# Performance work log

Measured on AMD Instinct MI355X. Metric: run time of the kernel, lower is better.

Reference implementation:

```python
import jax, jax.numpy as jnp
import numpy as np

B, C_IN, C_OUT, N, T = 32, 64, 192, 307, 24
DILATIONS = (1, 2)
O3 = C_OUT // 3  # out channels per branch


def setup_inputs() -> dict:
    key = jax.random.key(0)
    ks = iter(jax.random.split(key, 32))
    nrm = lambda shape: 0.05 * jax.random.normal(next(ks), shape, dtype=jnp.float32)
    return {
        "x": jax.random.normal(next(ks), (B, C_IN, N, T), dtype=jnp.float32),
        "adj": jax.random.randint(next(ks), (N, N), 0, 2, dtype=jnp.int32),
        "ln_g": jnp.ones((T,), jnp.float32),
        "ln_b": jnp.zeros((T,), jnp.float32),
        "res_W": nrm((C_OUT, C_IN)), "res_b": nrm((C_OUT,)),
        "ca_W1": nrm((T,)), "ca_W2": nrm((N, T)), "ca_W3": nrm((N,)),
        "cc_W": nrm((O3, C_IN)), "cc_b": nrm((O3,)),
        "ta_W1": nrm((N,)), "ta_W2": nrm((C_IN, N)), "ta_W3": nrm((C_IN,)),
        "tc_W0": nrm((O3, C_IN, 1, 2)), "tc_b0": nrm((O3,)),
        "tc_W1": nrm((O3, O3, 1, 2)), "tc_b1": nrm((O3,)),
        "ga_W1": nrm((T,)), "ga_W2": nrm((C_IN, T)), "ga_W3": nrm((C_IN,)),
        "g_W": nrm((O3, C_IN)),
    }


def layer_norm_lastdim(x, g, b, eps=1e-5):
    mu = jnp.mean(x, axis=-1, keepdims=True)
    var = jnp.var(x, axis=-1, keepdims=True)
    return (x - mu) * jax.lax.rsqrt(var + eps) * g + b


def conv1x1(x, W, b):
    # x: [B,C,N,T], W: [O,C]
    return jnp.einsum("oc,bcnt->bont", W, x) + b[None, :, None, None]


def c_attention(x, W1, W2, W3):
    # channel attention over C; x: [B,C,N,T]
    lhs = jnp.einsum("bcn,nt->bct", jnp.einsum("bcnt,t->bcn", x, W1), W2)  # [B,C,T]
    rhs = jnp.einsum("n,bcnt->bct", W3, x)                                  # [B,C,T]
    att = jax.nn.softmax(jnp.einsum("bct,bdt->bcd", lhs, rhs), axis=-1)     # [B,C,C]
    return jnp.einsum("bcd,bdnt->bcnt", att, x)


def t_attention(x, W1, W2, W3):
    # temporal attention over T; x: [B,C,N,T]
    lhs = jnp.einsum("bct,cn->btn", jnp.einsum("bcnt,n->bct", x, W1), W2)   # [B,T,N]
    rhs = jnp.einsum("c,bcnt->bnt", W3, x)                                   # [B,N,T]
    att = jax.nn.softmax(jnp.einsum("btn,bns->bts", lhs, rhs), axis=-1)      # [B,T,T]
    return jnp.einsum("bts,bcns->bcnt", att, x)


def g_attention(x, adj, W1, W2, W3):
    # graph (spatial) attention over N, masked by adjacency; x: [B,C,N,T]
    lhs = jnp.einsum("bcn,ct->bnt", jnp.einsum("bcnt,t->bcn", x, W1), W2)   # [B,N,T]
    rhs = jnp.einsum("c,bcnt->bnt", W3, x)                                   # [B,N,T]
    scores = jnp.einsum("bnt,bmt->bnm", lhs, rhs)                            # [B,N,N]
    scores = jnp.where(adj[None] > 0, scores, jnp.float32(-1e30))
    att = jax.nn.softmax(scores, axis=-1)
    return jnp.einsum("bnm,bcmt->bcnt", att, x)


def causal_conv(x, W, b, d):
    # Conv2d kernel [1,2], dilation [1,d], pad [0,d] + Chomp(d) == left-pad-only causal conv
    y = jax.lax.conv_general_dilated(
        x, W, window_strides=(1, 1), padding=((0, 0), (d, 0)),
        rhs_dilation=(1, d), dimension_numbers=("NCHW", "OIHW", "NCHW"))
    return y + b[None, :, None, None]


def meam_forward(x, adj, ln_g, ln_b, res_W, res_b, ca_W1, ca_W2, ca_W3, cc_W, cc_b,
                 ta_W1, ta_W2, ta_W3, tc_W0, tc_b0, tc_W1, tc_b1,
                 ga_W1, ga_W2, ga_W3, g_W):
    h = layer_norm_lastdim(x, ln_g, ln_b)
    # CACN branch: channel attention + 1x1 conv
    c_out = conv1x1(c_attention(h, ca_W1, ca_W2, ca_W3), cc_W, cc_b)
    # TACN branch: temporal attention + dilated causal convs
    t_out = t_attention(h, ta_W1, ta_W2, ta_W3)
    t_out = causal_conv(t_out, tc_W0, tc_b0, DILATIONS[0])
    t_out = causal_conv(t_out, tc_W1, tc_b1, DILATIONS[1])
    # GACN branch: graph attention + channel mixing
    g_out = jnp.einsum("oc,bcnt->bont", g_W, g_attention(h, adj, ga_W1, ga_W2, ga_W3))
    out = jnp.concatenate([c_out, t_out, g_out], axis=1)  # [B, C_OUT, N, T]
    return jax.nn.relu(out + conv1x1(x, res_W, res_b))


def reference(x, adj, ln_g, ln_b, res_W, res_b, ca_W1, ca_W2, ca_W3, cc_W, cc_b,
              ta_W1, ta_W2, ta_W3, tc_W0, tc_b0, tc_W1, tc_b1,
              ga_W1, ga_W2, ga_W3, g_W):
    return meam_forward(x, adj, ln_g, ln_b, res_W, res_b, ca_W1, ca_W2, ca_W3, cc_W, cc_b,
                        ta_W1, ta_W2, ta_W3, tc_W0, tc_b0, tc_W1, tc_b1,
                        ga_W1, ga_W2, ga_W3, g_W)
```

## Files before the change

### kernel.cpp

```cpp
#include <hip/hip_runtime.h>
#include <hip/hip_bf16.h>

#define BB 32
#define CC 64
#define NN 307
#define TT 24
#define CO 192
#define NT (NN*TT)
#define GO 1536

using bf16 = __hip_bfloat16;
typedef __attribute__((ext_vector_type(8))) short bf16x8;
typedef __attribute__((ext_vector_type(4))) float f32x4;

#define OFF_ln_g   0
#define OFF_ln_b   24
#define OFF_res_W  48
#define OFF_res_b  12336
#define OFF_ca_W1  12528
#define OFF_ca_W2  12552
#define OFF_ca_W3  19920
#define OFF_cc_W   20227
#define OFF_cc_b   24323
#define OFF_ta_W1  24387
#define OFF_ta_W2  24694
#define OFF_ta_W3  44342
#define OFF_tc_W0  44406
#define OFF_tc_b0  52598
#define OFF_tc_W1  52662
#define OFF_tc_b1  60854
#define OFF_ga_W1  60918
#define OFF_ga_W2  60942
#define OFF_ga_W3  62478
#define OFF_g_W    62542
#define W_TOTAL    66638

__device__ __forceinline__ float xload(const void* p, size_t i, int f) {
  return f ? ((const float*)p)[i] : __bfloat162float(((const bf16*)p)[i]);
}
__device__ __forceinline__ void ostore(void* p, size_t i, float v, int f) {
  if (f) ((float*)p)[i] = v; else ((bf16*)p)[i] = __float2bfloat16(v);
}
__device__ __forceinline__ float oload(const void* p, size_t i, int f) {
  return f ? ((const float*)p)[i] : __bfloat162float(((const bf16*)p)[i]);
}

__global__ void MEAM_44787918963464_kernel() {}

__global__ __launch_bounds__(256) void k_probe(const void* lng_raw, int* flag) {
  if (threadIdx.x == 0 && blockIdx.x == 0) {
    unsigned w = *(const unsigned*)lng_raw;
    *flag = (w == 0x3F800000u) ? 1 : 0;
  }
}

__global__ __launch_bounds__(256) void k_cvt_w(
    const void* p0, const void* p1, const void* p2, const void* p3,
    const void* p4, const void* p5, const void* p6, const void* p7,
    const void* p8, const void* p9, const void* p10, const void* p11,
    const void* p12, const void* p13, const void* p14, const void* p15,
    const void* p16, const void* p17, const void* p18, const void* p19,
    const int* flagp, float* dst) {
  int i = blockIdx.x*256 + threadIdx.x;
  if (i >= W_TOTAL) return;
  const void* ps[20] = {p0,p1,p2,p3,p4,p5,p6,p7,p8,p9,p10,p11,p12,p13,p14,p15,p16,p17,p18,p19};
  const int sz[20] = {24,24,12288,192,24,7368,307,4096,64,307,19648,64,8192,64,8192,64,24,1536,64,4096};
  int f = *flagp;
  int s = 0, base = 0;
  while (i >= base + sz[s]) { base += sz[s]; s++; }
  dst[i] = f ? ((const float*)ps[s])[i-base]
             : __bfloat162float(((const bf16*)ps[s])[i-base]);
}

__global__ __launch_bounds__(256) void k_prep_tc(const float* __restrict__ W,
    bf16* __restrict__ Ag, float* __restrict__ tb_bias) {
  int g = blockIdx.x*256 + threadIdx.x;
  if (g >= CC*CC) return;
  int pI = g >> 6, c = g & 63;
  const float* W0 = W + OFF_tc_W0;
  const float* b0 = W + OFF_tc_b0;
  const float* W1 = W + OFF_tc_W1;
  const float* b1 = W + OFF_tc_b1;
  const float* resW = W + OFF_res_W;
  const float* resb = W + OFF_res_b;
  float m0=0.f,m1=0.f,m2=0.f,m3=0.f, bb0=0.f, bb2=0.f;
  for (int o=0;o<CC;o++){
    float a1v = W1[(pI*CC+o)*2], b1v = W1[(pI*CC+o)*2+1];
    float a0v = W0[(o*CC+c)*2],  b0v = W0[(o*CC+c)*2+1];
    m0 += b1v*b0v; m1 += b1v*a0v; m2 += a1v*b0v; m3 += a1v*a0v;
    bb0 += b1v*b0[o]; bb2 += a1v*b0[o];
  }
  Ag[pI*320 + 0*64 + c] = __float2bfloat16(m0);
  Ag[pI*320 + 1*64 + c] = __float2bfloat16(m1);
  Ag[pI*320 + 2*64 + c] = __float2bfloat16(m2);
  Ag[pI*320 + 3*64 + c] = __float2bfloat16(m3);
  Ag[pI*320 + 4*64 + c] = __float2bfloat16(resW[(64+pI)*CC + c]);
  if (c == 0){
    tb_bias[pI]    = b1[pI] + bb0 + resb[64+pI];
    tb_bias[64+pI] = bb2;
  }
}

__global__ __launch_bounds__(256) void k_prep_A(const float* __restrict__ Mc,
    const float* __restrict__ W, bf16* __restrict__ Apre) {
  int idx = blockIdx.x*256 + threadIdx.x;
  if (idx >= BB*192*128) return;
  int b = idx / 24576;
  int rem = idx - b*24576;
  int p2 = rem >> 7, k = rem & 127;
  const float* resW = W + OFF_res_W;
  const float* gW   = W + OFF_g_W;
  float v;
  if (p2 < 64)       v = (k < 64) ? Mc[b*CC*CC + p2*CC + k] : resW[p2*CC + (k-64)];
  else if (p2 < 128) v = (k < 64) ? gW[(p2-64)*CC + k] : 0.f;
  else               v = (k < 64) ? 0.f : resW[p2*CC + (k-64)];
  Apre[idx] = __float2bfloat16(v);
}

__global__ __launch_bounds__(256) void k_ln(const void* __restrict__ x, const int* flagp,
    const float* __restrict__ W,
    float* __restrict__ mu_o, float* __restrict__ rs_o,
    float* __restrict__ xw1c, float* __restrict__ xw1g) {
  int r = blockIdx.x*256 + threadIdx.x;
  if (r >= BB*CC*NN) return;
  int f = *flagp;
  const float* lng  = W + OFF_ln_g;
  const float* lnb  = W + OFF_ln_b;
  const float* caW1 = W + OFF_ca_W1;
  const float* gaW1 = W + OFF_ga_W1;
  float v[TT];
  float mu = 0.f;
  for (int t=0;t<TT;t++){ v[t] = xload(x, (size_t)r*TT+t, f); mu += v[t]; }
  mu *= (1.f/TT);
  float var = 0.f;
  for (int t=0;t<TT;t++){ float d=v[t]-mu; var += d*d; }
  var *= (1.f/TT);
  float rs = rsqrtf(var + 1e-5f);
  float s1=0.f, s2=0.f;
  for (int t=0;t<TT;t++){
    float hv = (v[t]-mu)*rs*lng[t] + lnb[t];
    s1 += hv*caW1[t];
    s2 += hv*gaW1[t];
  }
  mu_o[r]=mu; rs_o[r]=rs; xw1c[r]=s1; xw1g[r]=s2;
}

__global__ __launch_bounds__(256) void k_prep_ct(const void* __restrict__ x, const int* flagp,
    const float* __restrict__ mu_a, const float* __restrict__ rs_a,
    const float* __restrict__ W, const float* __restrict__ xw1c,
    float* __restrict__ lhsc, float* __restrict__ rhsc, float* __restrict__ xw1t) {
  int i = blockIdx.x*256 + threadIdx.x;
  if (i >= BB*CC*TT) return;
  int f = *flagp;
  const float* lng  = W + OFF_ln_g;
  const float* lnb  = W + OFF_ln_b;
  const float* caW2 = W + OFF_ca_W2;
  const float* caW3 = W + OFF_ca_W3;
  const float* taW1 = W + OFF_ta_W1;
  int t = i % TT; int bc = i / TT;
  float gt = lng[t], bt = lnb[t];
  float l=0.f, rr=0.f, xt=0.f;
  for (int n=0;n<NN;n++){
    int row = bc*NN + n;
    float hv = (xload(x, (size_t)row*TT+t, f) - mu_a[row]) * rs_a[row] * gt + bt;
    l  += xw1c[row]*caW2[n*TT+t];
    rr += caW3[n]*hv;
    xt += taW1[n]*hv;
  }
  lhsc[i]=l; rhsc[i]=rr; xw1t[i]=xt;
}

__global__ __launch_bounds__(256) void k_prep_bn(const void* __restrict__ x, const int* flagp,
    const float* __restrict__ mu_a, const float* __restrict__ rs_a,
    const float* __restrict__ W, const float* __restrict__ xw1g,
    float* __restrict__ rhst, float* __restrict__ rhsg, float* __restrict__ lhsg) {
  int i = blockIdx.x*256 + threadIdx.x;
  if (i >= BB*NN*TT) return;
  int f = *flagp;
  const float* lng  = W + OFF_ln_g;
  const float* lnb  = W + OFF_ln_b;
  const float* taW3 = W + OFF_ta_W3;
  const float* gaW3 = W + OFF_ga_W3;
  const float* gaW2 = W + OFF_ga_W2;
  int t = i % TT; int n = (i/TT)%NN; int b = i/(NN*TT);
  float gt = lng[t], bt = lnb[t];
  float a=0.f,c2=0.f,d=0.f;
  for (int c=0;c<CC;c++){
    int row = (b*CC+c)*NN + n;
    float hv = (xload(x, (size_t)row*TT+t, f) - mu_a[row]) * rs_a[row] * gt + bt;
    a  += taW3[c]*hv;
    c2 += gaW3[c]*hv;
    d  += xw1g[row]*gaW2[c*TT+t];
  }
  rhst[i]=a; rhsg[i]=c2; lhsg[i]=d;
}

__global__ __launch_bounds__(256) void k_lhs_t(const float* __restrict__ xw1t,
    const float* __restrict__ W, float* __restrict__ lhst) {
  int i = blockIdx.x*256 + threadIdx.x;
  if (i >= BB*TT*NN) return;
  const float* taW2 = W + OFF_ta_W2;
  int n = i % NN; int t = (i/NN)%TT; int b = i/(TT*NN);
  float acc=0.f;
  for (int c=0;c<CC;c++)
    acc += xw1t[(b*CC+c)*TT+t]*taW2[c*NN+n];
  lhst[i]=acc;
}

__global__ __launch_bounds__(256) void k_att_c(const float* __restrict__ lhsc,
    const float* __restrict__ rhsc, const float* __restrict__ W,
    float* __restrict__ Mc) {
  int b = blockIdx.x; int tid = threadIdx.x;
  const float* ccW = W + OFF_cc_W;
  __shared__ float lc[CC*TT], rc[CC*TT], sc[CC*(CC+1)];
  for (int e=tid;e<CC*TT;e+=256){
    lc[e]=lhsc[b*CC*TT+e];
    rc[e]=rhsc[b*CC*TT+e];
  }
  __syncthreads();
  for (int e=tid;e<CC*CC;e+=256){
    int c=e>>6, d=e&63; float s=0.f;
    for (int t=0;t<TT;t++) s += lc[c*TT+t]*rc[d*TT+t];
    sc[c*(CC+1)+d]=s;
  }
  __syncthreads();
  if (tid<CC){
    float mx=-1e30f;
    for (int d=0;d<CC;d++) mx=fmaxf(mx, sc[tid*(CC+1)+d]);
    float sum=0.f;
    for (int d=0;d<CC;d++){ float e2=__expf(sc[tid*(CC+1)+d]-mx); sc[tid*(CC+1)+d]=e2; sum+=e2; }
    float inv=1.f/sum;
    for (int d=0;d<CC;d++) sc[tid*(CC+1)+d]*=inv;
  }
  __syncthreads();
  for (int e=tid;e<CC*CC;e+=256){
    int o=e>>6, d=e&63; float acc=0.f;
    for (int c=0;c<CC;c++) acc += ccW[o*CC+c]*sc[c*(CC+1)+d];
    Mc[b*CC*CC+e]=acc;
  }
}

__global__ __launch_bounds__(256) void k_att_t(const float* __restrict__ lhst,
    const float* __restrict__ rhst, float* __restrict__ attt) {
  int b=blockIdx.x, tid=threadIdx.x;
  __shared__ float sc[TT*TT];
  for (int e=tid;e<TT*TT;e+=256){
    int t=e/TT, s=e%TT;
    float acc=0.f;
    for (int n=0;n<NN;n++)
      acc += lhst[(b*TT+t)*NN+n]*rhst[(b*NN+n)*TT+s];
    sc[e]=acc;
  }
  __syncthreads();
  if (tid < TT){
    float mx=-1e30f;
    for (int s=0;s<TT;s++) mx=fmaxf(mx,sc[tid*TT+s]);
    float sum=0.f;
    for (int s=0;s<TT;s++){ float e=__expf(sc[tid*TT+s]-mx); sc[tid*TT+s]=e; sum+=e; }
    float inv=1.f/sum;
    for (int s=0;s<TT;s++) attt[b*TT*TT + tid*TT + s]=sc[tid*TT+s]*inv;
  }
}

__global__ __launch_bounds__(256) void k_scores_g(const float* __restrict__ lhsg,
    const float* __restrict__ rhsg, const int* __restrict__ adj,
    float* __restrict__ Sg) {
  int mt = blockIdx.x, nt = blockIdx.y, b = blockIdx.z;
  int n0 = nt*64, m0 = mt*64, tid = threadIdx.x;
  __shared__ unsigned short Lh[64*40], Ll[64*40], Rh[64*40], Rl[64*40];
  for (int e=tid; e<64*24; e+=256){
    int r=e/24, t=e-(e/24)*24;
    int gn=n0+r, gm=m0+r;
    float lv = (gn<NN)? lhsg[((size_t)b*NN+gn)*TT+t] : 0.f;
    float rv = (gm<NN)? rhsg[((size_t)b*NN+gm)*TT+t] : 0.f;
    bf16 lh=__float2bfloat16(lv); float lhf=__bfloat162float(lh);
    bf16 llo=__float2bfloat16(lv-lhf);
    bf16 rh=__float2bfloat16(rv); float rhf=__bfloat162float(rh);
    bf16 rlo=__float2bfloat16(rv-rhf);
    Lh[r*40+t]=*(unsigned short*)&lh; Ll[r*40+t]=*(unsigned short*)&llo;
    Rh[r*40+t]=*(unsigned short*)&rh; Rl[r*40+t]=*(unsigned short*)&rlo;
  }
  for (int e=tid; e<64*8; e+=256){
    int r=e>>3, t=24+(e&7);
    Lh[r*40+t]=0; Ll[r*40+t]=0; Rh[r*40+t]=0; Rl[r*40+t]=0;
  }
  __syncthreads();
  int lane=tid&63, w=tid>>6, q=lane>>4, lr=lane&15;
  bf16x8 ah = *(const bf16x8*)&Lh[(w*16+lr)*40 + q*8];
  bf16x8 al = *(const bf16x8*)&Ll[(w*16+lr)*40 + q*8];
  f32x4 z4={0.f,0.f,0.f,0.f};
  f32x4 acc[4]={z4,z4,z4,z4};
  #pragma unroll
  for (int ct=0;ct<4;ct++){
    bf16x8 bh = *(const bf16x8*)&Rh[(ct*16+lr)*40 + q*8];
    bf16x8 bl = *(const bf16x8*)&Rl[(ct*16+lr)*40 + q*8];
    acc[ct]=__builtin_amdgcn_mfma_f32_16x16x32_bf16(ah,bh,acc[ct],0,0,0);
    acc[ct]=__builtin_amdgcn_mfma_f32_16x16x32_bf16(ah,bl,acc[ct],0,0,0);
    acc[ct]=__builtin_amdgcn_mfma_f32_16x16x32_bf16(al,bh,acc[ct],0,0,0);
  }
  #pragma unroll
  for (int ct=0;ct<4;ct++){
    int m = m0 + ct*16 + lr;
    #pragma unroll
    for (int r=0;r<4;r++){
      int n = n0 + w*16 + q*4 + r;
      if (n<NN && m<NN){
        float s = acc[ct][r];
        if (adj[n*NN+m] <= 0) s = -1e30f;
        Sg[((size_t)b*NN+n)*NN+m] = s;
      }
    }
  }
}

__global__ __launch_bounds__(256) void k_smax_g(const float* __restrict__ Sg,
    bf16* __restrict__ attgh) {
  int b = blockIdx.y;
  int n = blockIdx.x*4 + (threadIdx.x>>6);
  int lane = threadIdx.x & 63;
  if (n >= NN) return;
  const float* row = Sg + ((size_t)b*NN+n)*NN;
  float v[5]; float mx = -1e30f;
  #pragma unroll
  for (int i=0;i<5;i++){
    int m = lane + i*64;
    v[i] = (m<NN)? row[m] : -1e30f;
    mx = fmaxf(mx, v[i]);
  }
  #pragma unroll
  for (int off=32; off; off>>=1) mx = fmaxf(mx, __shfl_xor(mx, off));
  float sum = 0.f;
  #pragma unroll
  for (int i=0;i<5;i++){
    int m = lane + i*64;
    float e = (m<NN)? __expf(v[i]-mx) : 0.f;
    v[i]=e; sum += e;
  }
  #pragma unroll
  for (int off=32; off; off>>=1) sum += __shfl_xor(sum, off);
  float inv = 1.f/sum;
  bf16* orow = attgh + ((size_t)b*NN+n)*NN;
  #pragma unroll
  for (int i=0;i<5;i++){
    int m = lane + i*64;
    if (m<NN) orow[m] = __float2bfloat16(v[i]*inv);
  }
}

__global__ __launch_bounds__(256) void k_hgc_mfma(
    const void* __restrict__ x, const int* flagp,
    const float* __restrict__ mu_a, const float* __restrict__ rs_a,
    const float* __restrict__ W, const bf16* __restrict__ Apre,
    bf16* __restrict__ hg, void* __restrict__ out) {
  int jt = blockIdx.x, b = blockIdx.y, tid = threadIdx.x;
  int f = *flagp;
  int j0 = jt*64;
  const float* lng = W + OFF_ln_g;
  const float* lnb = W + OFF_ln_b;
  const float* ccb = W + OFF_cc_b;
  const float* resb= W + OFF_res_b;
  __shared__ unsigned short Bs[64*128];

  {
    int c = tid >> 2, jg = tid & 3;
    float xv[16];
    int jbase = j0 + jg*16;
    size_t xoff = (size_t)(b*CC + c)*NT + jbase;
    if (jbase + 15 < NT) {
      if (f) {
        const float4* xp = (const float4*)((const float*)x + xoff);
        #pragma unroll
        for (int v=0; v<4; v++){ float4 q = xp[v]; xv[v*4]=q.x; xv[v*4+1]=q.y; xv[v*4+2]=q.z; xv[v*4+3]=q.w; }
      } else {
        const uint4* xp = (const uint4*)((const unsigned short*)x + xoff);
        #pragma unroll
        for (int v=0; v<2; v++){
          uint4 q = xp[v]; unsigned u[4]={q.x,q.y,q.z,q.w};
          #pragma unroll
          for (int kk2=0;kk2<4;kk2++){
            union{unsigned uu;float fl;} lo,hi;
            lo.uu=u[kk2]<<16; hi.uu=u[kk2]&0xffff0000u;
            xv[v*8+kk2*2]=lo.fl; xv[v*8+kk2*2+1]=hi.fl;
          }
        }
      }
    } else {
      #pragma unroll
      for (int i=0;i<16;i++){ int j=jbase+i; xv[i] = (j<NT)? xload(x, xoff+i, f) : 0.f; }
    }
    const float* mu_r = mu_a + (b*CC+c)*NN;
    const float* rs_r = rs_a + (b*CC+c)*NN;
    #pragma unroll
    for (int i=0;i<16;i++){
      int j = jbase + i;
      int jl = jg*16 + i;
      float hv = 0.f, xf = 0.f;
      if (j < NT){
        int n = j / 24, t = j - n*24;
        xf = xv[i];
        hv = (xf - mu_r[n]) * rs_r[n] * lng[t] + lnb[t];
      }
      int cs = c ^ ((jl&7)<<3);
      bf16 hb = __float2bfloat16(hv), xb = __float2bfloat16(xf);
      Bs[jl*128 + cs]      = *(unsigned short*)&hb;
      Bs[jl*128 + cs + 64] = *(unsigned short*)&xb;
    }
  }

  int lane = tid & 63, w = tid >> 6;
  int q = lane >> 4, lr = lane & 15;
  bf16x8 afo[4], afh[2], afr[2];
  {
    const unsigned short* Ab = (const unsigned short*)Apre + (size_t)b*24576;
    const unsigned short* r0 = Ab + (w*16 + lr)*128;
    #pragma unroll
    for (int kc=0;kc<4;kc++) afo[kc] = *(const bf16x8*)&r0[kc*32 + q*8];
    const unsigned short* r1 = Ab + (64 + w*16 + lr)*128;
    #pragma unroll
    for (int kc=0;kc<2;kc++) afh[kc] = *(const bf16x8*)&r1[kc*32 + q*8];
    const unsigned short* r2 = Ab + (128 + w*16 + lr)*128;
    #pragma unroll
    for (int kc=0;kc<2;kc++) afr[kc] = *(const bf16x8*)&r2[(kc+2)*32 + q*8];
  }
  f32x4 z4 = {0.f,0.f,0.f,0.f};
  f32x4 acco[4] = {z4,z4,z4,z4};
  f32x4 acch[4] = {z4,z4,z4,z4};
  f32x4 accr[4] = {z4,z4,z4,z4};
  __syncthreads();

  #pragma unroll
  for (int ct=0; ct<4; ct++){
    int jl = ct*16 + lr;
    int sw = ((jl&7)<<3);
    #pragma unroll
    for (int kc=0; kc<4; kc++){
      int ke = (kc*32 + q*8) ^ sw;
      bf16x8 bfr = *(const bf16x8*)&Bs[jl*128 + ke];
      acco[ct] = __builtin_amdgcn_mfma_f32_16x16x32_bf16(afo[kc], bfr, acco[ct], 0,0,0);
      if (kc < 2)
        acch[ct] = __builtin_amdgcn_mfma_f32_16x16x32_bf16(afh[kc], bfr, acch[ct], 0,0,0);
      else
        accr[ct] = __builtin_amdgcn_mfma_f32_16x16x32_bf16(afr[kc-2], bfr, accr[ct], 0,0,0);
    }
  }

  #pragma unroll
  for (int ct=0;ct<4;ct++){
    int jl = ct*16 + lr;
    int j = j0 + jl;
    if (j < NT){
      #pragma unroll
      for (int r=0;r<4;r++){
        int p2 = w*16 + q*4 + r;
        float v = acco[ct][r] + ccb[p2] + resb[p2];
        ostore(out, ((size_t)b*CO + p2)*NT + j, fmaxf(v,0.f), f);
      }
      int n = j/24, t2 = j - n*24;
      size_t hb2 = ((size_t)b*NN + n)*GO + t2;
      #pragma unroll
      for (int r=0;r<4;r++){
        int o = w*16 + q*4 + r;
        hg[hb2 + o*TT] = __float2bfloat16(acch[ct][r]);
      }
      #pragma unroll
      for (int r=0;r<4;r++){
        int p3 = w*16 + q*4 + r;
        ostore(out, ((size_t)b*CO + 128 + p3)*NT + j, accr[ct][r] + resb[128+p3], f);
      }
    }
  }
}

__global__ __launch_bounds__(256) void k_gemm_g(const bf16* __restrict__ attgh,
    const bf16* __restrict__ hg, const int* flagp, void* __restrict__ out) {
  int jt = blockIdx.x, nt = blockIdx.y, b = blockIdx.z;
  int tid = threadIdx.x;
  int f = *flagp;
  int n0 = nt*64, j0 = jt*64;
  __shared__ unsigned short As[64*72];
  __shared__ unsigned short Bs[64*72];
  int lane = tid & 63, w = tid >> 6;
  int q = lane >> 4, lr = lane & 15;
  f32x4 z4 = {0.f,0.f,0.f,0.f};
  f32x4 acc[4] = {z4,z4,z4,z4};
  const unsigned short* Ag = (const unsigned short*)attgh + (size_t)b*NN*NN;
  const unsigned short* Bg = (const unsigned short*)hg + (size_t)b*NN*GO;
  for (int m0=0;m0<NN;m0+=64){
    for (int u=tid; u<512; u+=256){
      int r=u>>3, kb=(u&7)*8;
      int gn=n0+r, gm=m0+kb;
      if (gn<NN && gm+7<NN){
        *(uint4*)&As[r*72+kb] = *(const uint4*)&Ag[(size_t)gn*NN + gm];
      } else {
        for (int i2=0;i2<8;i2++){
          int m=gm+i2;
          As[r*72+kb+i2] = (gn<NN && m<NN) ? Ag[(size_t)gn*NN+m] : 0;
        }
      }
    }
    for (int u=tid; u<512; u+=256){
      int m  = (u&7) | ((u>>6)<<3);
      int jb = ((u>>3)&7)*8;
      int gm = m0 + m;
      unsigned short s[8];
      if (gm < NN){
        *(uint4*)s = *(const uint4*)&Bg[(size_t)gm*GO + j0 + jb];
      } else {
        #pragma unroll
        for (int i2=0;i2<8;i2++) s[i2]=0;
      }
      #pragma unroll
      for (int i2=0;i2<8;i2++){
        int j = jb + i2;
        int col = ((((m>>3) ^ ((j>>3)&7)) << 3) | (m&7));
        Bs[j*72 + col] = s[i2];
      }
    }
    __syncthreads();
    #pragma unroll
    for (int kk=0;kk<64;kk+=32){
      bf16x8 af = *(const bf16x8*)&As[(w*16+lr)*72 + kk + q*8];
      #pragma unroll
      for (int ct=0;ct<4;ct++){
        int jrow = ct*16+lr;
        int kb = kk + q*8;
        int col = (((kb>>3) ^ ((jrow>>3)&7)) << 3);
        bf16x8 bfr = *(const bf16x8*)&Bs[jrow*72 + col];
        acc[ct] = __builtin_amdgcn_mfma_f32_16x16x32_bf16(af, bfr, acc[ct], 0,0,0);
      }
    }
    __syncthreads();
  }
  #pragma unroll
  for (int ct=0;ct<4;ct++){
    #pragma unroll
    for (int r=0;r<4;r++){
      int n = n0 + w*16 + q*4 + r;
      if (n >= NN) continue;
      int j = j0 + ct*16 + lr;
      int o = j/TT, t2 = j%TT;
      size_t idx = ((size_t)b*CO + 128 + o)*NT + (size_t)n*TT + t2;
      float v = acc[ct][r] + oload(out, idx, f);
      ostore(out, idx, fmaxf(v, 0.f), f);
    }
  }
}

__global__ __launch_bounds__(256) void k_cmix(const float* __restrict__ Mc,
    const void* __restrict__ x, const int* flagp,
    const float* __restrict__ mu_a, const float* __restrict__ rs_a,
    const float* __restrict__ W, void* __restrict__ out) {
  int jt=blockIdx.x, b=blockIdx.y, tid=threadIdx.x;
  int f = *flagp;
  int j0=jt*64;
  const float* lng = W + OFF_ln_g;
  const float* lnb = W + OFF_ln_b;
  const float* ccb = W + OFF_cc_b;
  __shared__ float Ms[CC*64];
  __shared__ float Hs[CC*64];
  for (int e=tid;e<CC*64;e+=256){
    int o=e&63, d=e>>6;
    Ms[e]=Mc[b*CC*CC + o*CC + d];
  }
  for (int e=tid;e<CC*64;e+=256){
    int d=e>>6, j=e&63; int jj=j0+j;
    float hv = 0.f;
    if (jj<NT){
      int n = jj/TT, t = jj%TT;
      int row = (b*CC+d)*NN + n;
      hv = (xload(x, (size_t)(b*CC+d)*NT + jj, f) - mu_a[row]) * rs_a[row] * lng[t] + lnb[t];
    }
    Hs[e]=hv;
  }
  __syncthreads();
  int ti=tid&15, tj=tid>>4;
  float acc[4][4]={};
  for (int d=0;d<CC;d++){
    float4 a4=*(const float4*)&Ms[d*64+ti*4];
    float4 b4=*(const float4*)&Hs[d*64+tj*4];
    float av[4]={a4.x,a4.y,a4.z,a4.w};
    float bv[4]={b4.x,b4.y,b4.z,b4.w};
    for (int i=0;i<4;i++)
      for (int j=0;j<4;j++) acc[i][j]+=av[i]*bv[j];
  }
  for (int i=0;i<4;i++){
    int o=ti*4+i; float bias=ccb[o];
    for (int j=0;j<4;j++){
      int jj=j0+tj*4+j;
      if (jj<NT)
        ostore(out, ((size_t)b*CO+o)*NT+jj, acc[i][j]+bias, f);
    }
  }
}

__global__ __launch_bounds__(256) void k_graph(const float* __restrict__ lhsg,
    const float* __restrict__ rhsg, const int* __restrict__ adj,
    const void* __restrict__ x, const int* flagp,
    const float* __restrict__ mu_a, const float* __restrict__ rs_a,
    const float* __restrict__ W, void* __restrict__ out) {
  int n = blockIdx.x, b = blockIdx.y, tid = threadIdx.x;
  int f = *flagp;
  const float* lng = W + OFF_ln_g;
  const float* lnb = W + OFF_ln_b;
  const float* gW  = W + OFF_g_W;
  __shared__ float ls[TT];
  __shared__ float sv[NN];
  __shared__ float red[256];
  __shared__ float wl[NN];
  __shared__ int   ml[NN];
  __shared__ int   cnt;
  __shared__ float z[CC*TT];
  __shared__ float Gs[CC*CC];
  __shared__ float gs[TT], bs[TT];
  if (tid < TT){
    ls[tid] = lhsg[(b*NN+n)*TT + tid];
    gs[tid] = lng[tid]; bs[tid] = lnb[tid];
  }
  for (int e=tid;e<CC*CC;e+=256) Gs[e]=gW[e];
  __syncthreads();
  float lmax = -1e30f;
  for (int m=tid;m<NN;m+=256){
    float s = -1e30f;
    if (adj[n*NN+m] > 0){
      const float* rr = rhsg + ((size_t)b*NN+m)*TT;
      float acc=0.f;
      for (int t=0;t<TT;t++) acc += ls[t]*rr[t];
      s = acc;
    }
    sv[m]=s; lmax=fmaxf(lmax,s);
  }
  red[tid]=lmax; __syncthreads();
  for (int k=128;k>0;k>>=1){ if (tid<k) red[tid]=fmaxf(red[tid],red[tid+k]); __syncthreads(); }
  float mx = red[0]; __syncthreads();
  float lsum=0.f;
  for (int m=tid;m<NN;m+=256){
    float e = (sv[m] > -1e29f) ? __expf(sv[m]-mx) : 0.f;
    sv[m]=e; lsum+=e;
  }
  red[tid]=lsum; __syncthreads();
  for (int k=128;k>0;k>>=1){ if (tid<k) red[tid]+=red[tid+k]; __syncthreads(); }
  float inv = 1.f/red[0];
  if (tid==0){
    int c=0;
    for (int m=0;m<NN;m++) if (sv[m]!=0.f){ ml[c]=m; wl[c]=sv[m]*inv; c++; }
    cnt=c;
  }
  __syncthreads();
  int K = cnt;
  {
    int c = tid>>2, tg = tid&3;
    float acc[6]={0,0,0,0,0,0};
    float s0 = 0.f;
    const float* mu_r = mu_a + (b*CC+c)*NN;
    const float* rs_r = rs_a + (b*CC+c)*NN;
    size_t xbase = (size_t)(b*CC+c)*NT;
    for (int k=0;k<K;k++){
      int m = ml[k];
      float wr = wl[k]*rs_r[m];
      s0 += wr*mu_r[m];
      size_t xm = xbase + m*TT + tg*6;
      for (int j=0;j<6;j++) acc[j] += wr*xload(x, xm+j, f);
    }
    for (int j=0;j<6;j++){
      int t = tg*6+j;
      z[c*TT+t] = gs[t]*(acc[j]-s0) + bs[t];
    }
  }
  __syncthreads();
  {
    int o = tid>>2, tg = tid&3;
    float acc[6]={0,0,0,0,0,0};
    for (int c=0;c<CC;c++){
      float gwv = Gs[o*CC+c];
      const float* zr = &z[c*TT + tg*6];
      for (int j=0;j<6;j++) acc[j] += gwv*zr[j];
    }
    size_t base = ((size_t)b*CO + 128 + o)*NT + n*TT + tg*6;
    for (int j=0;j<6;j++)
      ostore(out, base+j, acc[j], f);
  }
}

__global__ __launch_bounds__(256) void k_tbranch(const void* __restrict__ x, const int* flagp,
    const float* __restrict__ mu_a, const float* __restrict__ rs_a,
    const float* __restrict__ W, const float* __restrict__ attt,
    void* __restrict__ out, int fuse) {
  int chunk = blockIdx.x, b = blockIdx.y, tid = threadIdx.x;
  int f = *flagp;
  int n0 = chunk*4;
  const float* lng = W + OFF_ln_g;
  const float* lnb = W + OFF_ln_b;
  const float* W0  = W + OFF_tc_W0;
  const float* b0  = W + OFF_tc_b0;
  const float* W1  = W + OFF_tc_W1;
  const float* b1  = W + OFF_tc_b1;
  __shared__ float hs[256*25];
  __shared__ float at[TT*TT];
  for (int e=tid;e<CC*4*TT;e+=256){
    int c=e/(4*TT), rem=e%(4*TT), i=rem/TT, t=rem%TT;
    int n=n0+i;
    float hv=0.f;
    if (n<NN){
      int row=(b*CC+c)*NN+n;
      hv = (xload(x,(size_t)row*TT+t,f) - mu_a[row]) * rs_a[row] * lng[t] + lnb[t];
    }
    hs[(c*4+i)*25+t] = hv;
  }
  for (int e=tid;e<TT*TT;e+=256) at[e]=attt[b*TT*TT+e];
  __syncthreads();
  {
    float r[TT], o2[TT];
    float* myrow = &hs[tid*25];
    #pragma unroll
    for (int s=0;s<TT;s++) r[s]=myrow[s];
    for (int t=0;t<TT;t++){
      float a=0.f;
      #pragma unroll
      for (int s=0;s<TT;s++) a += at[t*TT+s]*r[s];
      o2[t]=a;
    }
    #pragma unroll
    for (int t=0;t<TT;t++) myrow[t]=o2[t];
  }
  __syncthreads();
  {
    int o = tid>>2, i = tid&3;
    float acc[TT];
    float bb = b0[o];
    for (int t=0;t<TT;t++) acc[t]=bb;
    for (int c=0;c<CC;c++){
      float wa = W0[(o*CC+c)*2], wb = W0[(o*CC+c)*2+1];
      const float* row = &hs[(c*4+i)*25];
      acc[0] += wb*row[0];
      #pragma unroll
      for (int t=1;t<TT;t++) acc[t] += wa*row[t-1] + wb*row[t];
    }
    __syncthreads();
    float* myrow = &hs[tid*25];
    #pragma unroll
    for (int t=0;t<TT;t++) myrow[t]=acc[t];
  }
  __syncthreads();
  {
    int o2 = tid>>2, i = tid&3;
    int n = n0+i;
    float acc[TT];
    float bb = b1[o2];
    for (int t=0;t<TT;t++) acc[t]=bb;
    for (int o=0;o<CC;o++){
      float wa = W1[(o2*CC+o)*2], wb = W1[(o2*CC+o)*2+1];
      const float* row = &hs[(o*4+i)*25];
      acc[0] += wb*row[0];
      acc[1] += wb*row[1];
      #pragma unroll
      for (int t=2;t<TT;t++) acc[t] += wa*row[t-2] + wb*row[t];
    }
    if (n<NN){
      size_t base = (((size_t)b*CO + 64 + o2)*NN + n)*TT;
      if (fuse){
        for (int t=0;t<TT;t++){
          float v = acc[t] + oload(out, base+t, f);
          ostore(out, base+t, fmaxf(v,0.f), f);
        }
      } else {
        for (int t=0;t<TT;t++) ostore(out, base+t, acc[t], f);
      }
    }
  }
}

__device__ __forceinline__ void tb_load_raw(const void* __restrict__ x, int f, int b, int c, int nn,
    float* h) {
  if (nn < NN) {
    size_t off = (size_t)(b*CC + c)*NT + (size_t)nn*TT;
    if (f) {
      const float4* xp = (const float4*)((const float*)x + off);
      #pragma unroll
      for (int v=0; v<6; v++){
        float4 q = xp[v];
        h[v*4+0]=q.x; h[v*4+1]=q.y; h[v*4+2]=q.z; h[v*4+3]=q.w;
      }
    } else {
      const uint4* xp = (const uint4*)((const unsigned short*)x + off);
      #pragma unroll
      for (int v=0; v<3; v++){
        uint4 q = xp[v];
        unsigned wsv[4] = {q.x,q.y,q.z,q.w};
        #pragma unroll
        for (int k=0;k<4;k++){
          union { unsigned u; float fl; } lo, hi;
          lo.u = wsv[k] << 16; hi.u = wsv[k] & 0xffff0000u;
          h[v*8 + k*2] = lo.fl; h[v*8 + k*2 + 1] = hi.fl;
        }
      }
    }
  } else {
    #pragma unroll
    for (int t=0;t<TT;t++) h[t]=0.f;
  }
}

__global__ __launch_bounds__(256) void k_tb_mfma(
    const void* __restrict__ x, const int* flagp,
    const float* __restrict__ mu_a, const float* __restrict__ rs_a,
    const float* __restrict__ W, const float* __restrict__ attt,
    const bf16* __restrict__ Agm, const float* __restrict__ tb_bias,
    void* __restrict__ out) {
  int chunk = blockIdx.x, b = blockIdx.y, tid = threadIdx.x;
  int f = *flagp;
  int n0 = chunk*8;
  const float* lng = W + OFF_ln_g;
  const float* lnb = W + OFF_ln_b;
  __shared__ unsigned short Bs[8*27*64];
  __shared__ unsigned short Xs[8*24*64];

  for (int e=tid; e<8*3*64; e+=256){
    int n = e/192, rem = e%192, s = rem>>6, cz = rem&63;
    Bs[((n*27+s)<<6) + cz] = 0;
  }

  int c  = tid & 63;
  int nA = tid >> 6;
  float h0[TT], h1[TT];
  tb_load_raw(x, f, b, c, n0+nA,   h0);
  tb_load_raw(x, f, b, c, n0+nA+4, h1);
  #pragma unroll
  for (int t=0;t<TT;t++){
    int cs = c ^ ((t&7)<<3);
    bf16 v0 = __float2bfloat16(h0[t]);
    bf16 v1 = __float2bfloat16(h1[t]);
    Xs[(nA*24+t)*64 + cs]     = *reinterpret_cast<unsigned short*>(&v0);
    Xs[((nA+4)*24+t)*64 + cs] = *reinterpret_cast<unsigned short*>(&v1);
  }
  {
    int nn0 = n0+nA, nn1 = n0+nA+4;
    if (nn0 < NN){
      int r = (b*CC+c)*NN + nn0; float mu = mu_a[r], rs = rs_a[r];
      #pragma unroll
      for (int t=0;t<TT;t++) h0[t] = (h0[t]-mu)*rs*lng[t] + lnb[t];
    }
    if (nn1 < NN){
      int r = (b*CC+c)*NN + nn1; float mu = mu_a[r], rs = rs_a[r];
      #pragma unroll
      for (int t=0;t<TT;t++) h1[t] = (h1[t]-mu)*rs*lng[t] + lnb[t];
    }
  }
  const float* att_b = attt + b*TT*TT;
  for (int t=0;t<TT;t++){
    float a0=0.f, a1=0.f;
    #pragma unroll
    for (int s=0;s<TT;s++){
      float wv = att_b[t*TT+s];
      a0 += wv*h0[s]; a1 += wv*h1[s];
    }
    int sI = t+3;
    int cs = c ^ ((sI&7)<<3);
    bf16 v0 = __float2bfloat16(a0);
    bf16 v1 = __float2bfloat16(a1);
    Bs[((nA*27+sI)<<6) + cs]     = *reinterpret_cast<unsigned short*>(&v0);
    Bs[(((nA+4)*27+sI)<<6) + cs] = *reinterpret_cast<unsigned short*>(&v1);
  }

  int lane = tid & 63, w = tid >> 6;
  int q = lane >> 4, lr = lane & 15;
  bf16x8 af[10];
  const unsigned short* Arow = (const unsigned short*)Agm + (size_t)(w*16+lr)*320;
  #pragma unroll
  for (int kc=0;kc<10;kc++)
    af[kc] = *(const bf16x8*)&Arow[kc*32 + q*8];

  f32x4 z4 = {0.f,0.f,0.f,0.f};
  f32x4 acc[12] = {z4,z4,z4,z4,z4,z4,z4,z4,z4,z4,z4,z4};
  __syncthreads();

  #pragma unroll
  for (int ct=0; ct<12; ct++){
    int col = ct*16 + lr;
    int nl = col/24, t = col - nl*24;
    #pragma unroll
    for (int kc=0;kc<8;kc++){
      int tap = kc>>1;
      int s = t + 3 - tap;
      int cb = ((kc&1)*32 + q*8) ^ ((s&7)<<3);
      bf16x8 bfr = *(const bf16x8*)&Bs[((nl*27+s)<<6) + cb];
      acc[ct] = __builtin_amdgcn_mfma_f32_16x16x32_bf16(af[kc], bfr, acc[ct], 0,0,0);
    }
    #pragma unroll
    for (int kc2=0;kc2<2;kc2++){
      int cb = (kc2*32 + q*8) ^ ((t&7)<<3);
      bf16x8 bfr = *(const bf16x8*)&Xs[(nl*24+t)*64 + cb];
      acc[ct] = __builtin_amdgcn_mfma_f32_16x16x32_bf16(af[8+kc2], bfr, acc[ct], 0,0,0);
    }
  }

  #pragma unroll
  for (int ct=0;ct<12;ct++){
    int col = ct*16 + lr;
    int nl = col/24, t = col - nl*24;
    int nn = n0 + nl;
    if (nn < NN){
      #pragma unroll
      for (int r=0;r<4;r++){
        int pI = w*16 + q*4 + r;
        size_t idx = ((size_t)b*CO + 64 + pI)*NT + (size_t)nn*TT + t;
        float v = acc[ct][r] + tb_bias[pI] + (t>=2 ? tb_bias[64+pI] : 0.f);
        ostore(out, idx, fmaxf(v, 0.f), f);
      }
    }
  }
}

__global__ __launch_bounds__(256) void k_res_final(const void* __restrict__ x, const int* flagp,
    const float* __restrict__ W, void* __restrict__ out) {
  int jt=blockIdx.x, ot=blockIdx.y, b=blockIdx.z; int tid=threadIdx.x;
  int f = *flagp;
  int j0=jt*64, o0=ot*64;
  const float* resW = W + OFF_res_W;
  const float* resb = W + OFF_res_b;
  __shared__ float Ws[CC*64];
  __shared__ float Xs[CC*64];
  for (int e=tid;e<CC*64;e+=256){
    int o=e&63, c=e>>6;
    Ws[e] = resW[(o0+o)*CC + c];
  }
  for (int e=tid;e<CC*64;e+=256){
    int c=e>>6, j=e&63; int jj=j0+j;
    Xs[e] = (jj<NT) ? xload(x, (size_t)(b*CC+c)*NT + jj, f) : 0.f;
  }
  __syncthreads();
  int ti=tid&15, tj=tid>>4;
  float acc[4][4]={};
  for (int k=0;k<CC;k++){
    float4 a4=*(const float4*)&Ws[k*64+ti*4];
    float4 b4=*(const float4*)&Xs[k*64+tj*4];
    float av[4]={a4.x,a4.y,a4.z,a4.w};
    float bv[4]={b4.x,b4.y,b4.z,b4.w};
    for (int i=0;i<4;i++)
      for (int j=0;j<4;j++) acc[i][j]+=av[i]*bv[j];
  }
  for (int i=0;i<4;i++){
    int o=o0+ti*4+i; float bias=resb[o];
    for (int j=0;j<4;j++){
      int jj=j0+tj*4+j;
      if (jj<NT){
        size_t idx=((size_t)b*CO+o)*NT+jj;
        float v = acc[i][j] + bias + oload(out, idx, f);
        ostore(out, idx, fmaxf(v,0.f), f);
      }
    }
  }
}

extern "C" void kernel_launch(void* const* d_in, const int* in_sizes, int n_in,
                              void* d_out, int out_size, void* d_ws, size_t ws_size,
                              hipStream_t stream) {
  const void* x     = d_in[0];
  const int*  adj   = (const int*)d_in[1];
  void* out = d_out;

  float* p = (float*)d_ws;
  int*   flagp = (int*)p; p += 4;
  float* Wf  = p; p += W_TOTAL;
  float* mu_a = p; p += (size_t)BB*CC*NN;
  float* rs_a = p; p += (size_t)BB*CC*NN;
  float* xw1c = p; p += (size_t)BB*CC*NN;
  float* xw1g = p; p += (size_t)BB*CC*NN;
  float* xw1t = p; p += (size_t)BB*CC*TT;
  float* lhsc = p; p += (size_t)BB*CC*TT;
  float* rhsc = p; p += (size_t)BB*CC*TT;
  float* rhst = p; p += (size_t)BB*NN*TT;
  float* rhsg = p; p += (size_t)BB*NN*TT;
  float* lhsg = p; p += (size_t)BB*NN*TT;
  float* lhst = p; p += (size_t)BB*TT*NN;
  float* attt = p; p += (size_t)BB*TT*TT;
  float* Mc   = p; p += (size_t)BB*CC*CC;
  bf16*  Agm  = (bf16*)p; p += 10240;
  float* tb_bias = p; p += 128;
  bf16*  Apre = (bf16*)p; p += (size_t)BB*192*128/2;
  float* Sg   = p; p += (size_t)BB*NN*NN + 16;
  bf16*  attgh = (bf16*)p; p += (size_t)BB*NN*NN/2 + 16;
  bf16*  hg   = (bf16*)p;
  size_t need = ((char*)(hg + (size_t)BB*NN*GO)) - (char*)d_ws;
  bool gemm_path = (ws_size >= need);

  k_probe<<<dim3(1), dim3(256), 0, stream>>>(d_in[2], flagp);
  k_cvt_w<<<dim3((W_TOTAL+255)/256), dim3(256), 0, stream>>>(
      d_in[2], d_in[3], d_in[4], d_in[5], d_in[6], d_in[7], d_in[8], d_in[9],
      d_in[10], d_in[11], d_in[12], d_in[13], d_in[14], d_in[15], d_in[16],
      d_in[17], d_in[18], d_in[19], d_in[20], d_in[21], flagp, Wf);
  k_ln<<<dim3((BB*CC*NN+255)/256), dim3(256), 0, stream>>>(x, flagp, Wf, mu_a, rs_a, xw1c, xw1g);
  k_prep_ct<<<dim3((BB*CC*TT+255)/256), dim3(256), 0, stream>>>(x, flagp, mu_a, rs_a, Wf, xw1c, lhsc, rhsc, xw1t);
  k_prep_bn<<<dim3((BB*NN*TT+255)/256), dim3(256), 0, stream>>>(x, flagp, mu_a, rs_a, Wf, xw1g, rhst, rhsg, lhsg);
  k_lhs_t<<<dim3((BB*TT*NN+255)/256), dim3(256), 0, stream>>>(xw1t, Wf, lhst);
  k_att_c<<<dim3(BB), dim3(256), 0, stream>>>(lhsc, rhsc, Wf, Mc);
  k_att_t<<<dim3(BB), dim3(256), 0, stream>>>(lhst, rhst, attt);
  if (gemm_path) {
    k_prep_tc<<<dim3(16), dim3(256), 0, stream>>>(Wf, Agm, tb_bias);
    k_prep_A<<<dim3((BB*192*128+255)/256), dim3(256), 0, stream>>>(Mc, Wf, Apre);
    int ntile = (NN+63)/64;
    k_scores_g<<<dim3(ntile, ntile, BB), dim3(256), 0, stream>>>(lhsg, rhsg, adj, Sg);
    k_smax_g<<<dim3((NN+3)/4, BB), dim3(256), 0, stream>>>(Sg, attgh);
    k_hgc_mfma<<<dim3((NT+63)/64, BB), dim3(256), 0, stream>>>(x, flagp, mu_a, rs_a, Wf, Apre, hg, out);
    k_tb_mfma<<<dim3((NN+7)/8, BB), dim3(256), 0, stream>>>(x, flagp, mu_a, rs_a, Wf, attt, Agm, tb_bias, out);
    k_gemm_g<<<dim3(GO/64, (NN+63)/64, BB), dim3(256), 0, stream>>>(attgh, hg, flagp, out);
  } else {
    k_cmix<<<dim3((NT+63)/64, BB), dim3(256), 0, stream>>>(Mc, x, flagp, mu_a, rs_a, Wf, out);
    k_graph<<<dim3(NN, BB), dim3(256), 0, stream>>>(lhsg, rhsg, adj, x, flagp, mu_a, rs_a, Wf, out);
    k_tbranch<<<dim3((NN+3)/4, BB), dim3(256), 0, stream>>>(x, flagp, mu_a, rs_a, Wf, attt, out, 0);
    k_res_final<<<dim3((NT+63)/64, 3, BB), dim3(256), 0, stream>>>(x, flagp, Wf, out);
  }
}
```

Before: 801.5 us.

## Vectorize LN loads, stage residual in bf16 scratch, simplify B-tile swizzle

k_ln now reads each 24-element row with wide float4/uint4 loads and fully unrolls its reductions instead of calling a per-element scalar loader. The graph-branch residual is written to a separate bf16 scratch buffer rather than to the output, so k_gemm_g reads half the bytes and skips a read-modify-write round trip on the output. The B-tile staging in k_gemm_g changes its thread-to-element mapping and swizzle arithmetic, which alters the global coalescing pattern and LDS bank behaviour. Storing the residual in bf16 lowers its precision and adds workspace.

After: 755.0 us. -5.8%, faster.

```diff
diff --git a/kernel.cpp b/kernel.cpp
--- a/kernel.cpp
+++ b/kernel.cpp
@@ -129,14 +129,34 @@
   const float* caW1 = W + OFF_ca_W1;
   const float* gaW1 = W + OFF_ga_W1;
   float v[TT];
+  if (f) {
+    const float4* xp = (const float4*)((const float*)x + (size_t)r*TT);
+    #pragma unroll
+    for (int i=0;i<6;i++){ float4 q = xp[i]; v[i*4]=q.x; v[i*4+1]=q.y; v[i*4+2]=q.z; v[i*4+3]=q.w; }
+  } else {
+    const uint4* xp = (const uint4*)((const unsigned short*)x + (size_t)r*TT);
+    #pragma unroll
+    for (int i=0;i<3;i++){
+      uint4 q = xp[i]; unsigned u[4]={q.x,q.y,q.z,q.w};
+      #pragma unroll
+      for (int k=0;k<4;k++){
+        union{unsigned uu;float fl;} lo,hi;
+        lo.uu=u[k]<<16; hi.uu=u[k]&0xffff0000u;
+        v[i*8+k*2]=lo.fl; v[i*8+k*2+1]=hi.fl;
+      }
+    }
+  }
   float mu = 0.f;
-  for (int t=0;t<TT;t++){ v[t] = xload(x, (size_t)r*TT+t, f); mu += v[t]; }
+  #pragma unroll
+  for (int t=0;t<TT;t++) mu += v[t];
   mu *= (1.f/TT);
   float var = 0.f;
+  #pragma unroll
   for (int t=0;t<TT;t++){ float d=v[t]-mu; var += d*d; }
   var *= (1.f/TT);
   float rs = rsqrtf(var + 1e-5f);
   float s1=0.f, s2=0.f;
+  #pragma unroll
   for (int t=0;t<TT;t++){
     float hv = (v[t]-mu)*rs*lng[t] + lnb[t];
     s1 += hv*caW1[t];
@@ -351,7 +371,7 @@
     const void* __restrict__ x, const int* flagp,
     const float* __restrict__ mu_a, const float* __restrict__ rs_a,
     const float* __restrict__ W, const bf16* __restrict__ Apre,
-    bf16* __restrict__ hg, void* __restrict__ out) {
+    bf16* __restrict__ hg, bf16* __restrict__ resg, void* __restrict__ out) {
   int jt = blockIdx.x, b = blockIdx.y, tid = threadIdx.x;
   int f = *flagp;
   int j0 = jt*64;
@@ -465,14 +485,15 @@
       #pragma unroll
       for (int r=0;r<4;r++){
         int p3 = w*16 + q*4 + r;
-        ostore(out, ((size_t)b*CO + 128 + p3)*NT + j, accr[ct][r] + resb[128+p3], f);
+        resg[((size_t)b*CC + p3)*NT + j] = __float2bfloat16(accr[ct][r] + resb[128+p3]);
       }
     }
   }
 }
 
 __global__ __launch_bounds__(256) void k_gemm_g(const bf16* __restrict__ attgh,
-    const bf16* __restrict__ hg, const int* flagp, void* __restrict__ out) {
+    const bf16* __restrict__ hg, const bf16* __restrict__ resg,
+    const int* flagp, void* __restrict__ out) {
   int jt = blockIdx.x, nt = blockIdx.y, b = blockIdx.z;
   int tid = threadIdx.x;
   int f = *flagp;
@@ -499,8 +520,7 @@
       }
     }
     for (int u=tid; u<512; u+=256){
-      int m  = (u&7) | ((u>>6)<<3);
-      int jb = ((u>>3)&7)*8;
+      int m = u>>3, jb = (u&7)*8;
       int gm = m0 + m;
       unsigned short s[8];
       if (gm < NN){
@@ -509,10 +529,11 @@
         #pragma unroll
         for (int i2=0;i2<8;i2++) s[i2]=0;
       }
+      int mb = m>>3, ml2 = m&7;
       #pragma unroll
       for (int i2=0;i2<8;i2++){
         int j = jb + i2;
-        int col = ((((m>>3) ^ ((j>>3)&7)) << 3) | (m&7));
+        int col = ((mb ^ (j>>3)) << 3) | ml2;
         Bs[j*72 + col] = s[i2];
       }
     }
@@ -524,7 +545,7 @@
       for (int ct=0;ct<4;ct++){
         int jrow = ct*16+lr;
         int kb = kk + q*8;
-        int col = (((kb>>3) ^ ((jrow>>3)&7)) << 3);
+        int col = (((kb>>3) ^ (jrow>>3)) << 3);
         bf16x8 bfr = *(const bf16x8*)&Bs[jrow*72 + col];
         acc[ct] = __builtin_amdgcn_mfma_f32_16x16x32_bf16(af, bfr, acc[ct], 0,0,0);
       }
@@ -540,7 +561,7 @@
       int j = j0 + ct*16 + lr;
       int o = j/TT, t2 = j%TT;
       size_t idx = ((size_t)b*CO + 128 + o)*NT + (size_t)n*TT + t2;
-      float v = acc[ct][r] + oload(out, idx, f);
+      float v = acc[ct][r] + __bfloat162float(resg[((size_t)b*CC + o)*NT + (size_t)n*TT + t2]);
       ostore(out, idx, fmaxf(v, 0.f), f);
     }
   }
@@ -979,6 +1000,7 @@
   bf16*  Apre = (bf16*)p; p += (size_t)BB*192*128/2;
   float* Sg   = p; p += (size_t)BB*NN*NN + 16;
   bf16*  attgh = (bf16*)p; p += (size_t)BB*NN*NN/2 + 16;
+  bf16*  resg = (bf16*)p; p += (size_t)BB*CC*NT/2 + 16;
   bf16*  hg   = (bf16*)p;
   size_t need = ((char*)(hg + (size_t)BB*NN*GO)) - (char*)d_ws;
   bool gemm_path = (ws_size >= need);
@@ -1000,9 +1022,9 @@
     int ntile = (NN+63)/64;
     k_scores_g<<<dim3(ntile, ntile, BB), dim3(256), 0, stream>>>(lhsg, rhsg, adj, Sg);
     k_smax_g<<<dim3((NN+3)/4, BB), dim3(256), 0, stream>>>(Sg, attgh);
-    k_hgc_mfma<<<dim3((NT+63)/64, BB), dim3(256), 0, stream>>>(x, flagp, mu_a, rs_a, Wf, Apre, hg, out);
+    k_hgc_mfma<<<dim3((NT+63)/64, BB), dim3(256), 0, stream>>>(x, flagp, mu_a, rs_a, Wf, Apre, hg, resg, out);
     k_tb_mfma<<<dim3((NN+7)/8, BB), dim3(256), 0, stream>>>(x, flagp, mu_a, rs_a, Wf, attt, Agm, tb_bias, out);
-    k_gemm_g<<<dim3(GO/64, (NN+63)/64, BB), dim3(256), 0, stream>>>(attgh, hg, flagp, out);
+    k_gemm_g<<<dim3(GO/64, (NN+63)/64, BB), dim3(256), 0, stream>>>(attgh, hg, resg, flagp, out);
   } else {
     k_cmix<<<dim3((NT+63)/64, BB), dim3(256), 0, stream>>>(Mc, x, flagp, mu_a, rs_a, Wf, out);
     k_graph<<<dim3(NN, BB), dim3(256), 0, stream>>>(lhsg, rhsg, adj, x, flagp, mu_a, rs_a, Wf, out);
```
